# Kernel tuning notes

Hardware: AMD Instinct MI355X
Metric: run time of the kernel (lower is better)

Reference implementation:

```python
import jax, jax.numpy as jnp
import numpy as np

B, IN_SIZE, IN_DIM = 16, 2048, 512
HEADS, OUT_SIZE = 4, 64
EPS = 0.1
MAX_ITER = 30
SIGMA = 0.1


def setup_inputs() -> dict:
    key = jax.random.key(0)
    k1, k2 = jax.random.split(key)
    x = jax.random.normal(k1, (B, IN_SIZE, IN_DIM), dtype=jnp.float32)
    stdv = 1.0 / np.sqrt(OUT_SIZE)
    weight = jax.random.uniform(k2, (HEADS, OUT_SIZE, IN_DIM), jnp.float32, -stdv, stdv)
    return {"x": x, "weight": weight}


def _position_filter(in_size, out_size, sigma):
    # 1-D gaussian position filter (image=False branch of get_position_filter)
    a = jnp.arange(0.0, in_size, dtype=jnp.float32)[:, None] / in_size
    b = jnp.arange(0.0, out_size, dtype=jnp.float32)[None, :] / out_size
    return jnp.exp(-(((a - b) / sigma) ** 2))  # (in_size, out_size)


def log_sinkhorn(K, iterations):
    """Log-domain Sinkhorn. K: (B, H, N, M) log-kernel.
    Row marginal a = 1/N (uniform, no mask). Scaling vectors are
    detached (envelope trick) before forming the transport plan,
    matching the original OTK implementation."""
    Bn, H, N, M = K.shape
    log_a = jnp.full((Bn, H, N), -jnp.log(jnp.float32(N)), dtype=K.dtype)
    u0 = jnp.zeros((Bn, H, N), K.dtype)
    v0 = jnp.zeros((Bn, H, M), K.dtype)

    def step(carry, _):
        u, v = carry
        Z = K + u[..., :, None] + v[..., None, :]
        u = log_a - jax.nn.logsumexp(Z, axis=-1)
        Z = K + u[..., :, None] + v[..., None, :]
        v = -jax.nn.logsumexp(Z, axis=-2)
        return (u, v), None

    (u, v), _ = jax.lax.scan(step, (u0, v0), None, length=iterations)
    u = jax.lax.stop_gradient(u)
    v = jax.lax.stop_gradient(v)
    return jnp.exp(K + u[..., :, None] + v[..., None, :])  # (B,H,N,M)


def reference(x, weight):
    # x: (B, N, D); weight: (H, M, D)
    pf = _position_filter(IN_SIZE, OUT_SIZE, SIGMA)  # (N, M)
    # euclidean cost via expansion (cdist)
    x2 = jnp.sum(x * x, axis=-1)                      # (B, N)
    w2 = jnp.sum(weight * weight, axis=-1)            # (H, M)
    xw = jnp.einsum('bnd,hmd->bhnm', x, weight)       # (B, H, N, M)
    C = jnp.sqrt(jnp.maximum(x2[:, None, :, None] + w2[None, :, None, :] - 2.0 * xw, 0.0))
    K = (-C / EPS) * pf[None, None]                   # position filter applied to log-kernel
    P = log_sinkhorn(K, MAX_ITER)                     # (B, H, N, M) transport plan
    # attn: (B, M, H, N) -> (B, M*H, N)
    attn = jnp.transpose(P, (0, 3, 1, 2)).reshape(B, OUT_SIZE * HEADS, IN_SIZE)
    out = jnp.matmul(attn, x)                         # (B, M*H, D)
    return out.reshape(B, OUT_SIZE, HEADS * IN_DIM)
```

## Files before the change

### kernel.cpp

```cpp
#include <hip/hip_runtime.h>
#include <hip/hip_fp16.h>


typedef _Float16 h2 __attribute__((ext_vector_type(2)));
typedef _Float16 h8 __attribute__((ext_vector_type(8)));
typedef float f4 __attribute__((ext_vector_type(4)));

#define NB 16
#define NN 2048
#define ND 512
#define NH 4
#define NM 64
#define NITER 30
#define EUSCALE 8.0f

static __device__ __forceinline__ float fdot2f(h2 a, h2 b, float c) {
#if __has_builtin(__builtin_amdgcn_fdot2)
  return __builtin_amdgcn_fdot2(a, b, c, false);
#else
  return (float)a[0] * (float)b[0] + (float)a[1] * (float)b[1] + c;
#endif
}

static __device__ __forceinline__ h2 pkrtz(float a, float b) {
  return __builtin_bit_cast(h2, __builtin_amdgcn_cvt_pkrtz(a, b));
}

static __device__ __forceinline__ h8 pack8(float4 a, float4 b) {
  h8 r;
  r[0] = (_Float16)a.x; r[1] = (_Float16)a.y; r[2] = (_Float16)a.z; r[3] = (_Float16)a.w;
  r[4] = (_Float16)b.x; r[5] = (_Float16)b.y; r[6] = (_Float16)b.z; r[7] = (_Float16)b.w;
  return r;
}

static __device__ __forceinline__ float sq4(float4 a) {
  return a.x * a.x + a.y * a.y + a.z * a.z + a.w * a.w;
}

__global__ __launch_bounds__(256) void k0_xt(const float* __restrict__ x,
                                             _Float16* __restrict__ xT) {
  __shared__ float tile[64][65];
  const int b = blockIdx.z;
  const int n0 = blockIdx.x * 64;
  const int d0 = blockIdx.y * 64;
  const int t = threadIdx.x;
  const int nr = t >> 2;
  const int ds = (t & 3) * 16;
  const float4* src = (const float4*)(x + ((size_t)(b * NN + n0 + nr) * ND + d0 + ds));
  float4 v0 = src[0], v1 = src[1], v2 = src[2], v3 = src[3];
  float vals[16] = {v0.x, v0.y, v0.z, v0.w, v1.x, v1.y, v1.z, v1.w,
                    v2.x, v2.y, v2.z, v2.w, v3.x, v3.y, v3.z, v3.w};
#pragma unroll
  for (int j = 0; j < 16; ++j) tile[ds + j][nr] = vals[j];
  __syncthreads();
  const int dr = t >> 2;
  const int ns = (t & 3) * 16;
  h8 o0, o1;
#pragma unroll
  for (int j = 0; j < 8; ++j) o0[j] = (_Float16)tile[dr][ns + j];
#pragma unroll
  for (int j = 0; j < 8; ++j) o1[j] = (_Float16)tile[dr][ns + 8 + j];
  _Float16* dst = xT + ((size_t)(b * ND + d0 + dr) * NN + n0 + ns);
  *(h8*)dst = o0;
  *(h8*)(dst + 8) = o1;
}

__global__ __launch_bounds__(512) void k1_buildE(const float* __restrict__ x,
                                                 const float* __restrict__ w,
                                                 _Float16* __restrict__ E) {
  __shared__ _Float16 Ah[128][72];
  __shared__ _Float16 Bh[256][72];
  __shared__ float x2s[128][4];
  __shared__ float w2s[256][2];
  __shared__ float x2r[128];
  __shared__ float w2r[256];

  const int b = blockIdx.y;
  const int n0 = blockIdx.x * 128;
  const int tid = threadIdx.x;
  const int lane = tid & 63;
  const int wv = tid >> 6;
  const int lrow = lane & 15;
  const int kq = lane >> 4;

  f4 acc[16];
#pragma unroll
  for (int i = 0; i < 16; ++i) acc[i] = (f4){0.f, 0.f, 0.f, 0.f};

  const int ar = tid >> 2, ac = (tid & 3) * 16;
  const int br = tid >> 1, bc = (tid & 1) * 32;
  const float* xsrc = x + ((size_t)(b * NN + n0 + ar) * ND + ac);
  const float* wsrc = w + ((size_t)br * ND + bc);
  float x2p = 0.f, w2p = 0.f;

  for (int kt = 0; kt < 8; ++kt) {
    {
      const float4* s4 = (const float4*)(xsrc + kt * 64);
      float4 a0 = s4[0], a1 = s4[1], a2 = s4[2], a3 = s4[3];
      x2p += sq4(a0) + sq4(a1) + sq4(a2) + sq4(a3);
      *(h8*)&Ah[ar][ac] = pack8(a0, a1);
      *(h8*)&Ah[ar][ac + 8] = pack8(a2, a3);
    }
    {
      const float4* s4 = (const float4*)(wsrc + kt * 64);
      float4 u0 = s4[0], u1 = s4[1], u2 = s4[2], u3 = s4[3];
      float4 u4 = s4[4], u5 = s4[5], u6 = s4[6], u7 = s4[7];
      w2p += sq4(u0) + sq4(u1) + sq4(u2) + sq4(u3)
           + sq4(u4) + sq4(u5) + sq4(u6) + sq4(u7);
      *(h8*)&Bh[br][bc] = pack8(u0, u1);
      *(h8*)&Bh[br][bc + 8] = pack8(u2, u3);
      *(h8*)&Bh[br][bc + 16] = pack8(u4, u5);
      *(h8*)&Bh[br][bc + 24] = pack8(u6, u7);
    }
    __syncthreads();
#pragma unroll
    for (int s = 0; s < 2; ++s) {
      h8 af = *(const h8*)&Ah[wv * 16 + lrow][s * 32 + kq * 8];
#pragma unroll
      for (int cf = 0; cf < 16; ++cf) {
        h8 bf = *(const h8*)&Bh[cf * 16 + lrow][s * 32 + kq * 8];
        acc[cf] = __builtin_amdgcn_mfma_f32_16x16x32_f16(af, bf, acc[cf], 0, 0, 0);
      }
    }
    __syncthreads();
  }

  x2s[ar][tid & 3] = x2p;
  w2s[br][tid & 1] = w2p;
  __syncthreads();
  if (tid < 128) {
    x2r[tid] = x2s[tid][0] + x2s[tid][1] + x2s[tid][2] + x2s[tid][3];
  } else if (tid < 384) {
    const int r = tid - 128;
    w2r[r] = w2s[r][0] + w2s[r][1];
  }
  __syncthreads();

#pragma unroll
  for (int cf = 0; cf < 16; ++cf) {
    const int mg = cf * 16 + lrow;
    const int hh = mg >> 6;
    const int m = mg & 63;
    const float w2v = w2r[mg];
    const float bm = (float)m * (1.0f / 64.0f);
    _Float16* Eb = E + ((size_t)(b * NH + hh) * NN) * NM;
#pragma unroll
    for (int j = 0; j < 4; ++j) {
      const int nl = wv * 16 + kq * 4 + j;
      const int n = n0 + nl;
      const float c2 = x2r[nl] + w2v - 2.0f * acc[cf][j];
      const float Cd = sqrtf(fmaxf(c2, 0.0f));
      const float tt = (float)n * (1.0f / 2048.0f) - bm;
      const float pf = __expf(-100.0f * tt * tt);
      const float Ev = __expf(-10.0f * Cd * pf);
      Eb[(size_t)n * NM + m] = (_Float16)Ev;
    }
  }
}

__global__ __launch_bounds__(512)
__attribute__((amdgpu_waves_per_eu(2, 2)))
void k2_sinkhorn(const _Float16* __restrict__ E,
                 _Float16* __restrict__ Pt) {
  const int bh = blockIdx.x;
  const int b = bh >> 2, h = bh & 3;
  const int tid = threadIdx.x;
  const int lane = tid & 63;

  __shared__ float evf[64];
  __shared__ __align__(16) h2 evh[32];
  __shared__ unsigned int pbuf[512];

  const _Float16* Ep = E + (size_t)bh * (NN * NM);

  h2 e[4][32];
#pragma unroll
  for (int i = 0; i < 4; ++i) {
    const uint4* src = (const uint4*)(Ep + (size_t)(4 * tid + i) * NM);
#pragma unroll
    for (int q = 0; q < 8; ++q) {
      uint4 v = src[q];
      e[i][q * 4 + 0] = __builtin_bit_cast(h2, v.x);
      e[i][q * 4 + 1] = __builtin_bit_cast(h2, v.y);
      e[i][q * 4 + 2] = __builtin_bit_cast(h2, v.z);
      e[i][q * 4 + 3] = __builtin_bit_cast(h2, v.w);
    }
  }

  float eu[4] = {1.f, 1.f, 1.f, 1.f};
  if (tid < 64) evf[tid] = 1.f;
  if (tid < 32) evh[tid] = pkrtz(1.f, 1.f);
  __syncthreads();

#pragma unroll 1
  for (int it = 0; it < NITER; ++it) {
    h2 evr[32];
    {
      const uint4* ev4 = (const uint4*)evh;
#pragma unroll
      for (int q8 = 0; q8 < 8; ++q8) {
        uint4 v = ev4[q8];
        evr[q8 * 4 + 0] = __builtin_bit_cast(h2, v.x);
        evr[q8 * 4 + 1] = __builtin_bit_cast(h2, v.y);
        evr[q8 * 4 + 2] = __builtin_bit_cast(h2, v.z);
        evr[q8 * 4 + 3] = __builtin_bit_cast(h2, v.w);
      }
    }
    float sa[4] = {0.f, 0.f, 0.f, 0.f};
    float sb[4] = {0.f, 0.f, 0.f, 0.f};
#pragma unroll
    for (int q = 0; q < 16; ++q) {
#pragma unroll
      for (int i = 0; i < 4; ++i) sa[i] = fdot2f(e[i][q], evr[q], sa[i]);
    }
#pragma unroll
    for (int q = 16; q < 32; ++q) {
#pragma unroll
      for (int i = 0; i < 4; ++i) sb[i] = fdot2f(e[i][q], evr[q], sb[i]);
    }
#pragma unroll
    for (int i = 0; i < 4; ++i) {
      eu[i] = 4.8828125e-4f * __builtin_amdgcn_rcpf(eu[i] * (sa[i] + sb[i]));
    }
    h2 eup[4];
#pragma unroll
    for (int i = 0; i < 4; ++i) {
      const float es = eu[i] * EUSCALE;
      eup[i] = pkrtz(es, es);
    }
    h2 tp[32];
#pragma unroll
    for (int q = 0; q < 32; ++q) {
      tp[q] = e[0][q] * eup[0] + e[1][q] * eup[1];
      tp[q] += e[2][q] * eup[2] + e[3][q] * eup[3];
    }
#pragma unroll
    for (int k = 0; k < 5; ++k) {
      const int nn = 32 >> k;
      const bool up = (lane >> k) & 1;
#pragma unroll
      for (int p = 0; p < (nn >> 1); ++p) {
        h2 keep = up ? tp[p + (nn >> 1)] : tp[p];
        h2 send = up ? tp[p] : tp[p + (nn >> 1)];
        int rv = __shfl_xor(__builtin_bit_cast(int, send), 1 << k, 64);
        tp[p] = keep + __builtin_bit_cast(h2, rv);
      }
    }
    pbuf[tid] = __builtin_bit_cast(unsigned int, tp[0]);
    __syncthreads();
    if (tid < 32) {
      const int j = tid;
      const int rev = ((j & 1) << 4) | ((j & 2) << 2) | (j & 4) | ((j & 8) >> 2) | ((j & 16) >> 4);
      float T0 = 0.f, T1 = 0.f;
#pragma unroll
      for (int wq = 0; wq < 8; ++wq) {
        h2 a = __builtin_bit_cast(h2, pbuf[wq * 64 + rev]);
        h2 c = __builtin_bit_cast(h2, pbuf[wq * 64 + rev + 32]);
        T0 += (float)a[0] + (float)c[0];
        T1 += (float)a[1] + (float)c[1];
      }
      const float e0 = evf[2 * j], e1 = evf[2 * j + 1];
      const float n0 = EUSCALE * __builtin_amdgcn_rcpf(e0 * T0);
      const float n1 = EUSCALE * __builtin_amdgcn_rcpf(e1 * T1);
      evf[2 * j] = n0;
      evf[2 * j + 1] = n1;
      evh[j] = pkrtz(n0, n1);
    }
    __syncthreads();
  }

  _Float16* Pb = Pt + ((size_t)(b * 256 + h)) * NN;
#pragma unroll
  for (int q = 0; q < 32; ++q) {
    const float ev0 = evf[2 * q];
    const float ev1 = evf[2 * q + 1];
    float a0[4], a1[4];
#pragma unroll
    for (int i = 0; i < 4; ++i) {
      a0[i] = (float)e[i][q][0] * eu[i] * ev0;
      a1[i] = (float)e[i][q][1] * eu[i] * ev1;
    }
    uint2 st0, st1;
    st0.x = __builtin_bit_cast(unsigned int, pkrtz(a0[0], a0[1]));
    st0.y = __builtin_bit_cast(unsigned int, pkrtz(a0[2], a0[3]));
    st1.x = __builtin_bit_cast(unsigned int, pkrtz(a1[0], a1[1]));
    st1.y = __builtin_bit_cast(unsigned int, pkrtz(a1[2], a1[3]));
    *(uint2*)(Pb + (size_t)(2 * q) * 4 * NN + 4 * tid) = st0;
    *(uint2*)(Pb + (size_t)(2 * q + 1) * 4 * NN + 4 * tid) = st1;
  }
}

__global__ __launch_bounds__(512) void k3_out(const _Float16* __restrict__ Pt,
                                              const _Float16* __restrict__ xT,
                                              float* __restrict__ out) {
  __shared__ _Float16 As[128][72];
  __shared__ _Float16 Bs[64][72];
  const int b = blockIdx.z;
  const int hf = blockIdx.y;
  const int dt = blockIdx.x;
  const int tid = threadIdx.x;
  const int lane = tid & 63;
  const int wv = tid >> 6;
  const int lrow = lane & 15;
  const int kq = lane >> 4;

  f4 acc[4];
#pragma unroll
  for (int i = 0; i < 4; ++i) acc[i] = (f4){0.f, 0.f, 0.f, 0.f};

  const int ar = tid >> 2, ac = (tid & 3) * 16;
  const int brd = tid >> 3, bn = (tid & 7) * 8;
  const _Float16* asrc = Pt + ((size_t)(b * 256 + hf * 128 + ar) * NN + ac);
  const _Float16* bsrc = xT + ((size_t)(b * ND + dt * 64 + brd) * NN + bn);

  for (int kt = 0; kt < 32; ++kt) {
    const int k0 = kt * 64;
    h8 a0 = *(const h8*)(asrc + k0);
    h8 a1 = *(const h8*)(asrc + k0 + 8);
    h8 bv = *(const h8*)(bsrc + k0);
    *(h8*)&As[ar][ac] = a0;
    *(h8*)&As[ar][ac + 8] = a1;
    *(h8*)&Bs[brd][bn] = bv;
    __syncthreads();
#pragma unroll
    for (int s = 0; s < 2; ++s) {
      h8 af = *(const h8*)&As[wv * 16 + lrow][s * 32 + kq * 8];
#pragma unroll
      for (int cf = 0; cf < 4; ++cf) {
        h8 bf = *(const h8*)&Bs[cf * 16 + lrow][s * 32 + kq * 8];
        acc[cf] = __builtin_amdgcn_mfma_f32_16x16x32_f16(af, bf, acc[cf], 0, 0, 0);
      }
    }
    __syncthreads();
  }
#pragma unroll
  for (int cf = 0; cf < 4; ++cf) {
    const int d = dt * 64 + cf * 16 + lrow;
#pragma unroll
    for (int j = 0; j < 4; ++j) {
      const int row = hf * 128 + wv * 16 + kq * 4 + j;
      out[(size_t)(b * 256 + row) * ND + d] = acc[cf][j];
    }
  }
}

extern "C" void kernel_launch(void* const* d_in, const int* in_sizes, int n_in,
                              void* d_out, int out_size, void* d_ws, size_t ws_size,
                              hipStream_t stream) {
  const float* x = (const float*)d_in[0];
  const float* w = (const float*)d_in[1];
  float* out = (float*)d_out;
  char* ws = (char*)d_ws;
  _Float16* xT = (_Float16*)ws;
  _Float16* E  = (_Float16*)(ws + (size_t)33554432);
  _Float16* Pt = (_Float16*)(ws + (size_t)50331648);

  k0_xt<<<dim3(32, 8, NB), 256, 0, stream>>>(x, xT);
  k1_buildE<<<dim3(16, NB), 512, 0, stream>>>(x, w, E);
  k2_sinkhorn<<<dim3(64), 512, 0, stream>>>(E, Pt);
  k3_out<<<dim3(8, 2, NB), 512, 0, stream>>>(Pt, xT, out);
}
```

Before: 172.0 us.

## Fuse transpose and cost-kernel launches; retile output GEMM with register prefetch

Merges the x-transpose kernel and the E-building kernel into one launch whose block index picks the role, using dynamic shared memory sized for the larger role. This removes a launch and lets the two independent jobs run at the same time. The output GEMM uses 256-thread blocks covering 64 rows, doubling the grid, and prefetches the next K-tile into registers while the current tile is consumed. In exchange, the fused kernel's 60 KB shared-memory request also applies to the light transpose blocks and may limit occupancy.

```diff
diff --git a/kernel.cpp b/kernel.cpp
--- a/kernel.cpp
+++ b/kernel.cpp
@@ -37,47 +37,57 @@
   return a.x * a.x + a.y * a.y + a.z * a.z + a.w * a.w;
 }
 
-__global__ __launch_bounds__(256) void k0_xt(const float* __restrict__ x,
-                                             _Float16* __restrict__ xT) {
-  __shared__ float tile[64][65];
-  const int b = blockIdx.z;
-  const int n0 = blockIdx.x * 64;
-  const int d0 = blockIdx.y * 64;
-  const int t = threadIdx.x;
-  const int nr = t >> 2;
-  const int ds = (t & 3) * 16;
-  const float4* src = (const float4*)(x + ((size_t)(b * NN + n0 + nr) * ND + d0 + ds));
-  float4 v0 = src[0], v1 = src[1], v2 = src[2], v3 = src[3];
-  float vals[16] = {v0.x, v0.y, v0.z, v0.w, v1.x, v1.y, v1.z, v1.w,
-                    v2.x, v2.y, v2.z, v2.w, v3.x, v3.y, v3.z, v3.w};
-#pragma unroll
-  for (int j = 0; j < 16; ++j) tile[ds + j][nr] = vals[j];
-  __syncthreads();
-  const int dr = t >> 2;
-  const int ns = (t & 3) * 16;
-  h8 o0, o1;
-#pragma unroll
-  for (int j = 0; j < 8; ++j) o0[j] = (_Float16)tile[dr][ns + j];
-#pragma unroll
-  for (int j = 0; j < 8; ++j) o1[j] = (_Float16)tile[dr][ns + 8 + j];
-  _Float16* dst = xT + ((size_t)(b * ND + d0 + dr) * NN + n0 + ns);
-  *(h8*)dst = o0;
-  *(h8*)(dst + 8) = o1;
-}
-
-__global__ __launch_bounds__(512) void k1_buildE(const float* __restrict__ x,
+__global__ __launch_bounds__(512) void k01_fused(const float* __restrict__ x,
                                                  const float* __restrict__ w,
+                                                 _Float16* __restrict__ xT,
                                                  _Float16* __restrict__ E) {
-  __shared__ _Float16 Ah[128][72];
-  __shared__ _Float16 Bh[256][72];
-  __shared__ float x2s[128][4];
-  __shared__ float w2s[256][2];
-  __shared__ float x2r[128];
-  __shared__ float w2r[256];
-
-  const int b = blockIdx.y;
-  const int n0 = blockIdx.x * 128;
+  extern __shared__ __align__(16) char smem[];
+  const int bid = blockIdx.x;
   const int tid = threadIdx.x;
+
+  if (bid < 2048) {
+    auto tile = (float(*)[65])smem;
+    const int sub = tid >> 8;
+    const int t = tid & 255;
+    const int xt = bid & 15;
+    const int dt = (bid >> 4) & 7;
+    const int b = bid >> 7;
+    const int n0 = (xt * 2 + sub) * 64;
+    const int d0 = dt * 64;
+    const int rbase = sub << 6;
+
+    const int nr = t >> 2;
+    const int ds = (t & 3) * 16;
+    const float4* src = (const float4*)(x + ((size_t)(b * NN + n0 + nr) * ND + d0 + ds));
+    float4 v0 = src[0], v1 = src[1], v2 = src[2], v3 = src[3];
+    float vals[16] = {v0.x, v0.y, v0.z, v0.w, v1.x, v1.y, v1.z, v1.w,
+                      v2.x, v2.y, v2.z, v2.w, v3.x, v3.y, v3.z, v3.w};
+#pragma unroll
+    for (int j = 0; j < 16; ++j) tile[rbase + ds + j][nr] = vals[j];
+    __syncthreads();
+    const int dr = t >> 2;
+    const int ns = (t & 3) * 16;
+    h8 o0, o1;
+#pragma unroll
+    for (int j = 0; j < 8; ++j) o0[j] = (_Float16)tile[rbase + dr][ns + j];
+#pragma unroll
+    for (int j = 0; j < 8; ++j) o1[j] = (_Float16)tile[rbase + dr][ns + 8 + j];
+    _Float16* dst = xT + ((size_t)(b * ND + d0 + dr) * NN + n0 + ns);
+    *(h8*)dst = o0;
+    *(h8*)(dst + 8) = o1;
+    return;
+  }
+
+  auto Ah  = (_Float16(*)[72])(smem);
+  auto Bh  = (_Float16(*)[72])(smem + 18432);
+  auto x2s = (float(*)[4])(smem + 55296);
+  auto w2s = (float(*)[2])(smem + 57344);
+  float* x2r = (float*)(smem + 59392);
+  float* w2r = (float*)(smem + 59904);
+
+  const int bid2 = bid - 2048;
+  const int b = bid2 >> 4;
+  const int n0 = (bid2 & 15) * 128;
   const int lane = tid & 63;
   const int wv = tid >> 6;
   const int lrow = lane & 15;
@@ -290,10 +300,10 @@
   }
 }
 
-__global__ __launch_bounds__(512) void k3_out(const _Float16* __restrict__ Pt,
+__global__ __launch_bounds__(256) void k3_out(const _Float16* __restrict__ Pt,
                                               const _Float16* __restrict__ xT,
                                               float* __restrict__ out) {
-  __shared__ _Float16 As[128][72];
+  __shared__ _Float16 As[64][72];
   __shared__ _Float16 Bs[64][72];
   const int b = blockIdx.z;
   const int hf = blockIdx.y;
@@ -309,19 +319,27 @@
   for (int i = 0; i < 4; ++i) acc[i] = (f4){0.f, 0.f, 0.f, 0.f};
 
   const int ar = tid >> 2, ac = (tid & 3) * 16;
-  const int brd = tid >> 3, bn = (tid & 7) * 8;
-  const _Float16* asrc = Pt + ((size_t)(b * 256 + hf * 128 + ar) * NN + ac);
-  const _Float16* bsrc = xT + ((size_t)(b * ND + dt * 64 + brd) * NN + bn);
+  const _Float16* asrc = Pt + ((size_t)(b * 256 + hf * 64 + ar) * NN + ac);
+  const _Float16* bsrc = xT + ((size_t)(b * ND + dt * 64 + ar) * NN + ac);
+
+  h8 a0 = *(const h8*)(asrc);
+  h8 a1 = *(const h8*)(asrc + 8);
+  h8 b0 = *(const h8*)(bsrc);
+  h8 b1 = *(const h8*)(bsrc + 8);
 
   for (int kt = 0; kt < 32; ++kt) {
-    const int k0 = kt * 64;
-    h8 a0 = *(const h8*)(asrc + k0);
-    h8 a1 = *(const h8*)(asrc + k0 + 8);
-    h8 bv = *(const h8*)(bsrc + k0);
     *(h8*)&As[ar][ac] = a0;
     *(h8*)&As[ar][ac + 8] = a1;
-    *(h8*)&Bs[brd][bn] = bv;
-    __syncthreads();
+    *(h8*)&Bs[ar][ac] = b0;
+    *(h8*)&Bs[ar][ac + 8] = b1;
+    __syncthreads();
+    if (kt < 31) {
+      const int k0 = (kt + 1) * 64;
+      a0 = *(const h8*)(asrc + k0);
+      a1 = *(const h8*)(asrc + k0 + 8);
+      b0 = *(const h8*)(bsrc + k0);
+      b1 = *(const h8*)(bsrc + k0 + 8);
+    }
 #pragma unroll
     for (int s = 0; s < 2; ++s) {
       h8 af = *(const h8*)&As[wv * 16 + lrow][s * 32 + kq * 8];
@@ -338,7 +356,7 @@
     const int d = dt * 64 + cf * 16 + lrow;
 #pragma unroll
     for (int j = 0; j < 4; ++j) {
-      const int row = hf * 128 + wv * 16 + kq * 4 + j;
+      const int row = hf * 64 + wv * 16 + kq * 4 + j;
       out[(size_t)(b * 256 + row) * ND + d] = acc[cf][j];
     }
   }
@@ -355,8 +373,7 @@
   _Float16* E  = (_Float16*)(ws + (size_t)33554432);
   _Float16* Pt = (_Float16*)(ws + (size_t)50331648);
 
-  k0_xt<<<dim3(32, 8, NB), 256, 0, stream>>>(x, xT);
-  k1_buildE<<<dim3(16, NB), 512, 0, stream>>>(x, w, E);
-  k2_sinkhorn<<<dim3(64), 512, 0, stream>>>(E, Pt);
-  k3_out<<<dim3(8, 2, NB), 512, 0, stream>>>(Pt, xT, out);
-}
+  k01_fused<<<2304, 512, 60928, stream>>>(x, w, xT, E);
+  k2_sinkhorn<<<64, 512, 0, stream>>>(E, Pt);
+  k3_out<<<dim3(8, 4, NB), 256, 0, stream>>>(Pt, xT, out);
+}
```

Measured after the change: 161.8 us. 5.9% less time.
